# Kernel optimization log

Measured on AMD Instinct MI355X. Metric: run time of the kernel, lower is better.

## Reference

```python
import jax, jax.numpy as jnp
import numpy as np
import math

N_USR = 50000
N_ENT = 100000
D = 64
N_REL = 16
E = 1_000_000
EI = 500_000
N_HEADS = 2


def setup_inputs() -> dict:
    key = jax.random.key(0)
    ks = jax.random.split(key, 9)
    user_emb = jax.random.normal(ks[0], (N_USR, D), jnp.float32) * 0.1
    entity_emb = jax.random.normal(ks[1], (N_ENT, D), jnp.float32) * 0.1
    edge_index = jax.random.randint(ks[2], (2, E), 0, N_ENT, dtype=jnp.int32)
    edge_type = jax.random.randint(ks[3], (E,), 1, N_REL + 1, dtype=jnp.int32)  # values in [1, N_REL]
    inter_u = jax.random.randint(ks[4], (EI,), 0, N_USR, dtype=jnp.int32)
    inter_i = jax.random.randint(ks[5], (EI,), 0, N_ENT, dtype=jnp.int32)
    inter_edge = jnp.stack([inter_u, inter_i], axis=0)
    inter_edge_w = jax.random.uniform(ks[6], (EI,), jnp.float32)
    relation_emb = jax.random.normal(ks[7], (N_REL, D), jnp.float32) * 0.1
    W_Q = jax.random.normal(ks[8], (D, D), jnp.float32) * 0.1
    return {
        'layers_num': 2,
        'user_emb': user_emb,
        'entity_emb': entity_emb,
        'inter_edge': inter_edge,
        'inter_edge_w': inter_edge_w,
        'edge_index': edge_index,
        'edge_type': edge_type,
        'relation_emb': relation_emb,
        'W_Q': W_Q,
    }


def _scatter_softmax(scores, idx, n_segments):
    # scores: [E, H]; softmax over edges sharing the same head index
    m = jax.ops.segment_max(scores, idx, num_segments=n_segments)  # [n, H]
    ex = jnp.exp(scores - m[idx])
    denom = jax.ops.segment_sum(ex, idx, num_segments=n_segments)
    return ex / denom[idx]


def reference(layers_num, user_emb, entity_emb, inter_edge, inter_edge_w, edge_index, edge_type, relation_emb, W_Q):
    n_entities = entity_emb.shape[0]
    n_users = user_emb.shape[0]
    d = entity_emb.shape[1]
    h = N_HEADS
    dk = d // h
    head, tail = edge_index[0], edge_index[1]
    iu, ii = inter_edge[0], inter_edge[1]

    def agg_layer(u_emb, e_emb):
        rel = relation_emb[edge_type - 1]                                # [E, d]
        query = (e_emb[head] @ W_Q).reshape(-1, h, dk)                   # [E, h, dk]
        key = (e_emb[tail] @ W_Q).reshape(-1, h, dk) * rel.reshape(-1, h, dk)
        score = (query * key).sum(-1) / math.sqrt(dk)                    # [E, h]
        attn = _scatter_softmax(score, head, n_entities)                 # [E, h]
        value = (e_emb[tail] * rel).reshape(-1, h, dk)                   # [E, h, dk]
        entity_agg = (value * attn[:, :, None]).reshape(-1, d)           # [E, d]
        entity_agg = jax.ops.segment_sum(entity_agg, head, num_segments=n_entities)
        # F.normalize (L2, eps=1e-12)
        norm = jnp.sqrt(jnp.sum(entity_agg * entity_agg, axis=1, keepdims=True))
        entity_agg = entity_agg / jnp.maximum(norm, 1e-12)
        item_agg = inter_edge_w[:, None] * e_emb[ii]                      # [Ei, d]
        user_agg = jax.ops.segment_sum(item_agg, iu, num_segments=n_users)
        return entity_agg, user_agg

    user_embs = [user_emb]
    entity_embs = [entity_emb]
    u, e = user_emb, entity_emb
    for _ in range(layers_num):
        e, u = agg_layer(u, e)
        user_embs.append(u)
        entity_embs.append(e)
    user_out = jnp.mean(jnp.stack(user_embs, axis=1), axis=1)
    entity_out = jnp.mean(jnp.stack(entity_embs, axis=1), axis=1)
    return (user_out, entity_out)
```

## Files before the change

### kernel.cpp

```cpp
#include <hip/hip_runtime.h>
#include <hip/hip_fp16.h>
#include <math.h>

#define N_USR 50000
#define N_ENT 100000
#define DIM   64
#define NE    1000000
#define NEI   500000

#define BKW   250
#define EBK   400
#define UBK   200
#define CAP   3456
#define KCH   4096
#define NBA_E 245
#define NBA_U 123

#define NBE_B 6250
#define NBU_B 3125

__device__ __forceinline__ __half2 pick_lo(unsigned a, unsigned b) {
    unsigned r = __builtin_amdgcn_perm(b, a, 0x05040100u);
    return *(__half2*)&r;
}
__device__ __forceinline__ __half2 pick_hi(unsigned a, unsigned b) {
    unsigned r = __builtin_amdgcn_perm(b, a, 0x07060302u);
    return *(__half2*)&r;
}

template <int CTRL>
__device__ __forceinline__ float dpp_add(float x) {
    int y = __builtin_amdgcn_update_dpp(0, __builtin_bit_cast(int, x),
                                        CTRL, 0xF, 0xF, true);
    return x + __builtin_bit_cast(float, y);
}

__device__ __forceinline__ int swz16_maxi(int x) {
    int t = __builtin_amdgcn_ds_swizzle(x, 0x401F);
    return max(x, t);
}

typedef _Float16 fp16x2 __attribute__((ext_vector_type(2)));
__device__ __forceinline__ float dot2(__half2 a, __half2 b, float c) {
#if __has_builtin(__builtin_amdgcn_fdot2)
    return __builtin_amdgcn_fdot2(__builtin_bit_cast(fp16x2, a),
                                  __builtin_bit_cast(fp16x2, b), c, false);
#else
    __half2 m = __hmul2(a, b);
    return c + __low2float(m) + __high2float(m);
#endif
}

__device__ __forceinline__ float exp2_fast(float x) {
#if __has_builtin(__builtin_amdgcn_exp2f)
    return __builtin_amdgcn_exp2f(x);
#else
    return exp2f(x);
#endif
}

__global__ __launch_bounds__(256) void k_gemm(const float* __restrict__ Emat,
                                              const float* __restrict__ WQ,
                                              unsigned int* __restrict__ Gu,
                                              __half* __restrict__ Eh, int nrows) {
    int lane = threadIdx.x & 63;
    int wid  = (int)((blockIdx.x * 256 + threadIdx.x) >> 6);
    int nw   = (int)((gridDim.x * 256) >> 6);
    float w[64];
#pragma unroll
    for (int k = 0; k < 64; k++) w[k] = WQ[k * 64 + lane];
    for (int row = wid; row < nrows; row += nw) {
        int rowu = __builtin_amdgcn_readfirstlane(row);
        const float* er = Emat + (size_t)rowu * DIM;
        float acc = 0.f;
#pragma unroll
        for (int k = 0; k < 64; k++) acc = fmaf(er[k], w[k], acc);
        float ecol = er[lane];
        unsigned short hp = __half_as_ushort(__float2half(acc));
        unsigned short he = __half_as_ushort(__float2half(ecol));
        Gu[(size_t)rowu * 64 + lane] = (unsigned int)hp | ((unsigned int)he << 16);
        Eh[(size_t)rowu * 64 + lane] = __ushort_as_half(he);
    }
}

__global__ __launch_bounds__(256) void k_bucketA(const int* __restrict__ eidx,
                                                 const int* __restrict__ etype,
                                                 const int* __restrict__ inter,
                                                 const float* __restrict__ w,
                                                 int* __restrict__ gcnt,
                                                 int* __restrict__ ebuf,
                                                 int2* __restrict__ ubuf) {
    __shared__ int ch[EBK];
    int tid = threadIdx.x;
    int blk = blockIdx.x;
    for (int j = tid; j < EBK; j += 256) ch[j] = 0;
    __syncthreads();
    if (blk < NBA_E) {
        int lo = blk * KCH, hi = min(lo + KCH, NE);
        for (int i = lo + tid; i < hi; i += 256)
            atomicAdd(&ch[eidx[i] / BKW], 1);
        __syncthreads();
        for (int j = tid; j < EBK; j += 256)
            ch[j] = atomicAdd(&gcnt[j], ch[j]);
        __syncthreads();
        for (int i = lo + tid; i < hi; i += 256) {
            int head = eidx[i];
            int b    = head / BKW;
            int pos  = atomicAdd(&ch[b], 1);
            if (pos < CAP)
                ebuf[b * CAP + pos] = eidx[NE + i] | ((etype[i] - 1) << 20)
                                      | ((head - b * BKW) << 24);
        }
    } else {
        int ub = blk - NBA_E;
        int lo = ub * KCH, hi = min(lo + KCH, NEI);
        for (int i = lo + tid; i < hi; i += 256)
            atomicAdd(&ch[inter[i] / BKW], 1);
        __syncthreads();
        for (int j = tid; j < UBK; j += 256)
            ch[j] = atomicAdd(&gcnt[EBK + j], ch[j]);
        __syncthreads();
        for (int i = lo + tid; i < hi; i += 256) {
            int u   = inter[i];
            int b   = u / BKW;
            int pos = atomicAdd(&ch[b], 1);
            if (pos < CAP)
                ubuf[b * CAP + pos] = make_int2(inter[NEI + i] | ((u - b * BKW) << 24),
                                                __float_as_int(w[i]));
        }
    }
}

__global__ __launch_bounds__(512) void k_bucketB(const int* __restrict__ gcnt,
                                                 const int* __restrict__ ebuf,
                                                 const int2* __restrict__ ubuf,
                                                 int2* __restrict__ off2_e,
                                                 int* __restrict__ edges,
                                                 int2* __restrict__ off2_u,
                                                 int2* __restrict__ iw) {
    __shared__ int h[512];
    __shared__ int cur[512];
    __shared__ int s0[CAP];
    __shared__ int s1[CAP];
    int tid = threadIdx.x;
    int b   = blockIdx.x;
    bool isU = (b >= EBK);
    int lb   = isU ? b - EBK : b;
    int n    = min(gcnt[b], CAP);
    int base = lb * BKW;
    int gbase = lb * CAP;
    h[tid] = 0;
    __syncthreads();
    if (!isU) {
        const int* src = ebuf + (size_t)lb * CAP;
        for (int q = tid; q < n; q += 512) atomicAdd(&h[((unsigned)src[q]) >> 24], 1);
        __syncthreads();
        int v = h[tid];
        for (int d = 1; d < 512; d <<= 1) {
            int x = (tid >= d) ? h[tid - d] : 0;
            __syncthreads();
            h[tid] += x;
            __syncthreads();
        }
        int excl = h[tid] - v;
        cur[tid] = excl;
        if (tid < BKW) off2_e[base + tid] = make_int2(gbase + excl, v);
        __syncthreads();
        for (int q = tid; q < n; q += 512) {
            int x = src[q];
            int r = atomicAdd(&cur[((unsigned)x) >> 24], 1);
            s0[r] = x;
        }
        __syncthreads();
        for (int q = tid; q < n; q += 512) edges[gbase + q] = s0[q] & 0xFFFFFF;
    } else {
        const int2* src = ubuf + (size_t)lb * CAP;
        for (int q = tid; q < n; q += 512) atomicAdd(&h[((unsigned)src[q].x) >> 24], 1);
        __syncthreads();
        int v = h[tid];
        for (int d = 1; d < 512; d <<= 1) {
            int x = (tid >= d) ? h[tid - d] : 0;
            __syncthreads();
            h[tid] += x;
            __syncthreads();
        }
        int excl = h[tid] - v;
        cur[tid] = excl;
        if (tid < BKW) off2_u[base + tid] = make_int2(gbase + excl, v);
        __syncthreads();
        for (int q = tid; q < n; q += 512) {
            int2 x = src[q];
            int r = atomicAdd(&cur[((unsigned)x.x) >> 24], 1);
            s0[r] = x.x;
            s1[r] = x.y;
        }
        __syncthreads();
        for (int q = tid; q < n; q += 512)
            iw[gbase + q] = make_int2(s0[q] & 0xFFFFFF, s1[q]);
    }
}

#define ENT_GATHER(G, R, PK)                                                  \
    {                                                                         \
        G = *(const uint4*)(Gu + (size_t)(unsigned)(PK & 0xFFFFF) * 64 + 4 * dq); \
        R = *(const uint2*)(srel2 + ((((unsigned)PK >> 20) << 5) + dq2));     \
    }

#define ENT_BODY(G, R, KK)                                                    \
    {                                                                         \
        __half2 ra = *(__half2*)&(R).x;                                       \
        __half2 rb = *(__half2*)&(R).y;                                       \
        float sc = dot2(q2a, __hmul2(pick_lo((G).x, (G).y), ra), 0.f);        \
        sc = dot2(q2b, __hmul2(pick_lo((G).z, (G).w), rb), sc);               \
        sc = dpp_add<0xB1>(sc);                                               \
        sc = dpp_add<0x4E>(sc);                                               \
        sc = dpp_add<0x141>(sc);                                              \
        float ex = ((KK) < deg) ? exp2_fast(sc) : 0.f;                        \
        den += ex;                                                            \
        __half2 va = __hmul2(pick_hi((G).x, (G).y), ra);                      \
        __half2 vb = __hmul2(pick_hi((G).z, (G).w), rb);                      \
        acc0 = fmaf(ex, __low2float(va), acc0);                               \
        acc1 = fmaf(ex, __high2float(va), acc1);                              \
        acc2 = fmaf(ex, __low2float(vb), acc2);                               \
        acc3 = fmaf(ex, __high2float(vb), acc3);                              \
    }

__device__ __forceinline__ void ent_path(const unsigned int* __restrict__ Gu,
                                         const unsigned int* srel2,
                                         const int2* __restrict__ off2,
                                         const int* __restrict__ edges,
                                         float* __restrict__ enext,
                                         float* __restrict__ out_ent,
                                         const float* __restrict__ base0,
                                         int mode, int row0, int lane) {
    int grp  = lane >> 4;
    int dq   = lane & 15;
    int dq2  = 2 * dq;
    int row  = row0 + grp;
    uint4 qg = *(const uint4*)(Gu + (size_t)row * 64 + 4 * dq);
    const __half2 qs = __float2half2_rn(0.17677669529663687f * 1.44269504088896340f);
    __half2 q2a = __hmul2(pick_lo(qg.x, qg.y), qs);
    __half2 q2b = __hmul2(pick_lo(qg.z, qg.w), qs);
    int2 od = off2[row];
    int lo = od.x, deg = od.y;
    int km = swz16_maxi(deg);
    km = max(km, __shfl_xor(km, 32, 64));
    float acc0 = 0.f, acc1 = 0.f, acc2 = 0.f, acc3 = 0.f, den = 0.f;
    for (int k = 0; k < km; k += 8) {
        const int* ep = edges + lo + k;
        int r0 = ep[0], r1 = ep[1], r2 = ep[2], r3 = ep[3];
        int r4 = ep[4], r5 = ep[5], r6 = ep[6], r7 = ep[7];
        int p0 = (k + 0 < deg) ? r0 : 0;
        int p1 = (k + 1 < deg) ? r1 : 0;
        int p2 = (k + 2 < deg) ? r2 : 0;
        int p3 = (k + 3 < deg) ? r3 : 0;
        int p4 = (k + 4 < deg) ? r4 : 0;
        int p5 = (k + 5 < deg) ? r5 : 0;
        int p6 = (k + 6 < deg) ? r6 : 0;
        int p7 = (k + 7 < deg) ? r7 : 0;
        bool c1 = (k + 1 < km), c2 = (k + 2 < km), c3 = (k + 3 < km);
        bool c4 = (k + 4 < km), c5 = (k + 5 < km), c6 = (k + 6 < km);
        bool c7 = (k + 7 < km);
        uint4 G0, G1, G2, G3, G4, G5, G6, G7;
        uint2 R0, R1, R2, R3, R4, R5, R6, R7;
        ENT_GATHER(G0, R0, p0);
        if (c1) ENT_GATHER(G1, R1, p1);
        if (c2) ENT_GATHER(G2, R2, p2);
        if (c3) ENT_GATHER(G3, R3, p3);
        if (c4) ENT_GATHER(G4, R4, p4);
        if (c5) ENT_GATHER(G5, R5, p5);
        if (c6) ENT_GATHER(G6, R6, p6);
        if (c7) ENT_GATHER(G7, R7, p7);
        ENT_BODY(G0, R0, k);
        if (c1) ENT_BODY(G1, R1, k + 1);
        if (c2) ENT_BODY(G2, R2, k + 2);
        if (c3) ENT_BODY(G3, R3, k + 3);
        if (c4) ENT_BODY(G4, R4, k + 4);
        if (c5) ENT_BODY(G5, R5, k + 5);
        if (c6) ENT_BODY(G6, R6, k + 6);
        if (c7) ENT_BODY(G7, R7, k + 7);
    }
    float rden = (den > 0.f) ? 1.0f / den : 0.f;
    float rx = acc0 * rden, ry = acc1 * rden, rz = acc2 * rden, rw = acc3 * rden;
    float ss = rx * rx + ry * ry + rz * rz + rw * rw;
    ss = dpp_add<0xB1>(ss);
    ss = dpp_add<0x4E>(ss);
    ss = dpp_add<0x141>(ss);
    ss = dpp_add<0x140>(ss);
    float inv = 1.0f / fmaxf(sqrtf(ss), 1e-12f);
    size_t idx = (size_t)row * 16 + dq;
    float4 y = make_float4(rx * inv, ry * inv, rz * inv, rw * inv);
    if (mode == 0) {
        ((float4*)enext)[idx] = y;
        float4 b0 = ((const float4*)base0)[idx];
        ((float4*)out_ent)[idx] = make_float4(b0.x + y.x, b0.y + y.y,
                                              b0.z + y.z, b0.w + y.w);
    } else {
        float4 o = ((float4*)out_ent)[idx];
        ((float4*)out_ent)[idx] = make_float4((o.x + y.x) * (1.0f / 3.0f),
                                              (o.y + y.y) * (1.0f / 3.0f),
                                              (o.z + y.z) * (1.0f / 3.0f),
                                              (o.w + y.w) * (1.0f / 3.0f));
    }
}

#define USR_BODY(G, V, KK)                                                    \
    {                                                                         \
        float cw = ((KK) < deg) ? __int_as_float((V).y) : 0.f;                \
        __half2 h0 = *(__half2*)&(G).x;                                       \
        __half2 h1 = *(__half2*)&(G).y;                                       \
        acc0 = fmaf(cw, __low2float(h0), acc0);                               \
        acc1 = fmaf(cw, __high2float(h0), acc1);                              \
        acc2 = fmaf(cw, __low2float(h1), acc2);                               \
        acc3 = fmaf(cw, __high2float(h1), acc3);                              \
    }

__device__ __forceinline__ void usr_path(const unsigned int* __restrict__ Eh2,
                                         const int2* __restrict__ off2,
                                         const int2* __restrict__ iw,
                                         float* __restrict__ out_user,
                                         const float* __restrict__ base0,
                                         int mode, int row0, int lane) {
    int grp  = lane >> 4;
    int dq   = lane & 15;
    int dq2  = 2 * dq;
    int row  = row0 + grp;
    int2 od = off2[row];
    int lo = od.x, deg = od.y;
    int km = swz16_maxi(deg);
    km = max(km, __shfl_xor(km, 32, 64));
    float acc0 = 0.f, acc1 = 0.f, acc2 = 0.f, acc3 = 0.f;
    for (int k = 0; k < km; k += 8) {
        const int2* vp = iw + lo + k;
        int2 v0 = vp[0], v1 = vp[1], v2 = vp[2], v3 = vp[3];
        int2 v4 = vp[4], v5 = vp[5], v6 = vp[6], v7 = vp[7];
        int t0 = (k + 0 < deg) ? v0.x : 0;
        int t1 = (k + 1 < deg) ? v1.x : 0;
        int t2 = (k + 2 < deg) ? v2.x : 0;
        int t3 = (k + 3 < deg) ? v3.x : 0;
        int t4 = (k + 4 < deg) ? v4.x : 0;
        int t5 = (k + 5 < deg) ? v5.x : 0;
        int t6 = (k + 6 < deg) ? v6.x : 0;
        int t7 = (k + 7 < deg) ? v7.x : 0;
        bool c1 = (k + 1 < km), c2 = (k + 2 < km), c3 = (k + 3 < km);
        bool c4 = (k + 4 < km), c5 = (k + 5 < km), c6 = (k + 6 < km);
        bool c7 = (k + 7 < km);
        uint2 g0, g1, g2, g3, g4, g5, g6, g7;
        g0 = *(const uint2*)(Eh2 + (size_t)t0 * 32 + dq2);
        if (c1) g1 = *(const uint2*)(Eh2 + (size_t)t1 * 32 + dq2);
        if (c2) g2 = *(const uint2*)(Eh2 + (size_t)t2 * 32 + dq2);
        if (c3) g3 = *(const uint2*)(Eh2 + (size_t)t3 * 32 + dq2);
        if (c4) g4 = *(const uint2*)(Eh2 + (size_t)t4 * 32 + dq2);
        if (c5) g5 = *(const uint2*)(Eh2 + (size_t)t5 * 32 + dq2);
        if (c6) g6 = *(const uint2*)(Eh2 + (size_t)t6 * 32 + dq2);
        if (c7) g7 = *(const uint2*)(Eh2 + (size_t)t7 * 32 + dq2);
        USR_BODY(g0, v0, k);
        if (c1) USR_BODY(g1, v1, k + 1);
        if (c2) USR_BODY(g2, v2, k + 2);
        if (c3) USR_BODY(g3, v3, k + 3);
        if (c4) USR_BODY(g4, v4, k + 4);
        if (c5) USR_BODY(g5, v5, k + 5);
        if (c6) USR_BODY(g6, v6, k + 6);
        if (c7) USR_BODY(g7, v7, k + 7);
    }
    size_t idx = (size_t)row * 16 + dq;
    if (mode == 0) {
        float4 b0 = ((const float4*)base0)[idx];
        ((float4*)out_user)[idx] = make_float4(b0.x + acc0, b0.y + acc1,
                                               b0.z + acc2, b0.w + acc3);
    } else {
        float4 o = ((float4*)out_user)[idx];
        ((float4*)out_user)[idx] = make_float4((o.x + acc0) * (1.0f / 3.0f),
                                               (o.y + acc1) * (1.0f / 3.0f),
                                               (o.z + acc2) * (1.0f / 3.0f),
                                               (o.w + acc3) * (1.0f / 3.0f));
    }
}

__global__ __launch_bounds__(256) void k_agg(const unsigned int* __restrict__ Gu,
                                             const unsigned int* __restrict__ Eh2,
                                             const float* __restrict__ rel,
                                             const int2* __restrict__ off2_e,
                                             const int* __restrict__ edges,
                                             const int2* __restrict__ off2_u,
                                             const int2* __restrict__ iw,
                                             float* __restrict__ enext,
                                             float* __restrict__ out_ent,
                                             const float* __restrict__ ent0,
                                             float* __restrict__ out_user,
                                             const float* __restrict__ usr0,
                                             int mode) {
    __shared__ unsigned int srel2[16 * 32];
    int tid = threadIdx.x;
    int b   = blockIdx.x;
    int g   = b / 3;
    int r   = b - 3 * g;
    int lane = tid & 63;
    int wv   = tid >> 6;
    if (r < 2) {
        for (int i = tid; i < 16 * 32; i += 256) {
            float2 rp = ((const float2*)rel)[i];
            __half2 h = __floats2half2_rn(rp.x, rp.y);
            srel2[i] = *(unsigned int*)&h;
        }
        __syncthreads();
        int row0 = (2 * g + r) * 16 + wv * 4;
        ent_path(Gu, srel2, off2_e, edges, enext, out_ent, ent0, mode, row0, lane);
    } else {
        int row0 = g * 16 + wv * 4;
        usr_path(Eh2, off2_u, iw, out_user, usr0, mode, row0, lane);
    }
}

extern "C" void kernel_launch(void* const* d_in, const int* in_sizes, int n_in,
                              void* d_out, int out_size, void* d_ws, size_t ws_size,
                              hipStream_t stream) {
    const float* user_emb   = (const float*)d_in[1];
    const float* entity_emb = (const float*)d_in[2];
    const int*   inter_edge = (const int*)d_in[3];
    const float* inter_w    = (const float*)d_in[4];
    const int*   edge_index = (const int*)d_in[5];
    const int*   edge_type  = (const int*)d_in[6];
    const float* rel_emb    = (const float*)d_in[7];
    const float* wq         = (const float*)d_in[8];

    float* out      = (float*)d_out;
    float* out_user = out;
    float* out_ent  = out + (size_t)N_USR * DIM;

    const size_t SZ_E = (size_t)N_ENT * DIM * sizeof(float);
    char* ws = (char*)d_ws;
    size_t o = 0;
#define ALIGN16() o = (o + 15) & ~(size_t)15
    unsigned int* Gu = (unsigned int*)(ws + o); o += (size_t)N_ENT * 64 * 4;
    __half* Eh     = (__half*)(ws + o); o += (size_t)N_ENT * 64 * 2;
    float* eA      = (float*)(ws + o); o += SZ_E;
    ALIGN16();
    int*   edges   = (int*)  (ws + o); o += ((size_t)EBK * CAP + CAP + 16) * 4;
    ALIGN16();
    int2*  off2_e  = (int2*) (ws + o); o += (size_t)N_ENT * 8;
    ALIGN16();
    int2*  iw      = (int2*) (ws + o); o += ((size_t)UBK * CAP + CAP + 16) * 8;
    int2*  off2_u  = (int2*) (ws + o); o += (size_t)N_USR * 8;
    ALIGN16();
    int*   ebuf    = (int*)  (ws + o); o += (size_t)EBK * CAP * 4;
    ALIGN16();
    int2*  ubuf    = (int2*) (ws + o); o += (size_t)UBK * CAP * 8;
    int*   gcnt    = (int*)  (ws + o); o += (EBK + UBK) * 4;

    hipMemsetAsync(gcnt, 0, (EBK + UBK) * 4, stream);
    k_bucketA<<<NBA_E + NBA_U, 256, 0, stream>>>(edge_index, edge_type,
                                                 inter_edge, inter_w, gcnt,
                                                 ebuf, ubuf);
    k_bucketB<<<EBK + UBK, 512, 0, stream>>>(gcnt, ebuf, ubuf,
                                             off2_e, edges, off2_u, iw);

    const int layers = 2;
    for (int L = 0; L < layers; L++) {
        const float* ecur = (L == 0) ? entity_emb : eA;
        k_gemm<<<1536, 256, 0, stream>>>(ecur, wq, Gu, Eh, N_ENT);
        k_agg<<<NBE_B + NBU_B, 256, 0, stream>>>(Gu, (const unsigned int*)Eh, rel_emb,
                                                 off2_e, edges, off2_u, iw,
                                                 eA, out_ent, entity_emb,
                                                 out_user, user_emb, L);
    }
}
```

Before: 310.6 us.

## Halve agg block size, unroll by four with software-prefetched edge indices

```diff
diff --git a/kernel.cpp b/kernel.cpp
--- a/kernel.cpp
+++ b/kernel.cpp
@@ -8,16 +8,16 @@
 #define NE    1000000
 #define NEI   500000
 
-#define BKW   250
-#define EBK   400
-#define UBK   200
-#define CAP   3456
+#define BKW   125
+#define EBK   800
+#define UBK   400
+#define CAP   1664
 #define KCH   4096
 #define NBA_E 245
 #define NBA_U 123
 
-#define NBE_B 6250
-#define NBU_B 3125
+#define NBE_B 12500
+#define NBU_B 6250
 
 __device__ __forceinline__ __half2 pick_lo(unsigned a, unsigned b) {
     unsigned r = __builtin_amdgcn_perm(b, a, 0x05040100u);
@@ -246,39 +246,28 @@
     int km = swz16_maxi(deg);
     km = max(km, __shfl_xor(km, 32, 64));
     float acc0 = 0.f, acc1 = 0.f, acc2 = 0.f, acc3 = 0.f, den = 0.f;
-    for (int k = 0; k < km; k += 8) {
-        const int* ep = edges + lo + k;
-        int r0 = ep[0], r1 = ep[1], r2 = ep[2], r3 = ep[3];
-        int r4 = ep[4], r5 = ep[5], r6 = ep[6], r7 = ep[7];
-        int p0 = (k + 0 < deg) ? r0 : 0;
-        int p1 = (k + 1 < deg) ? r1 : 0;
-        int p2 = (k + 2 < deg) ? r2 : 0;
-        int p3 = (k + 3 < deg) ? r3 : 0;
-        int p4 = (k + 4 < deg) ? r4 : 0;
-        int p5 = (k + 5 < deg) ? r5 : 0;
-        int p6 = (k + 6 < deg) ? r6 : 0;
-        int p7 = (k + 7 < deg) ? r7 : 0;
+    const int* ep = edges + lo;
+    int r0 = ep[0], r1 = ep[1], r2 = ep[2], r3 = ep[3];
+    for (int k = 0; k < km; k += 4) {
+        int e0v = r0, e1v = r1, e2v = r2, e3v = r3;
+        if (k + 4 < km) {
+            r0 = ep[k + 4]; r1 = ep[k + 5]; r2 = ep[k + 6]; r3 = ep[k + 7];
+        }
+        int p0 = (k + 0 < deg) ? e0v : 0;
+        int p1 = (k + 1 < deg) ? e1v : 0;
+        int p2 = (k + 2 < deg) ? e2v : 0;
+        int p3 = (k + 3 < deg) ? e3v : 0;
         bool c1 = (k + 1 < km), c2 = (k + 2 < km), c3 = (k + 3 < km);
-        bool c4 = (k + 4 < km), c5 = (k + 5 < km), c6 = (k + 6 < km);
-        bool c7 = (k + 7 < km);
-        uint4 G0, G1, G2, G3, G4, G5, G6, G7;
-        uint2 R0, R1, R2, R3, R4, R5, R6, R7;
+        uint4 G0, G1, G2, G3;
+        uint2 R0, R1, R2, R3;
         ENT_GATHER(G0, R0, p0);
         if (c1) ENT_GATHER(G1, R1, p1);
         if (c2) ENT_GATHER(G2, R2, p2);
         if (c3) ENT_GATHER(G3, R3, p3);
-        if (c4) ENT_GATHER(G4, R4, p4);
-        if (c5) ENT_GATHER(G5, R5, p5);
-        if (c6) ENT_GATHER(G6, R6, p6);
-        if (c7) ENT_GATHER(G7, R7, p7);
         ENT_BODY(G0, R0, k);
         if (c1) ENT_BODY(G1, R1, k + 1);
         if (c2) ENT_BODY(G2, R2, k + 2);
         if (c3) ENT_BODY(G3, R3, k + 3);
-        if (c4) ENT_BODY(G4, R4, k + 4);
-        if (c5) ENT_BODY(G5, R5, k + 5);
-        if (c6) ENT_BODY(G6, R6, k + 6);
-        if (c7) ENT_BODY(G7, R7, k + 7);
     }
     float rden = (den > 0.f) ? 1.0f / den : 0.f;
     float rx = acc0 * rden, ry = acc1 * rden, rz = acc2 * rden, rw = acc3 * rden;
@@ -304,9 +293,9 @@
     }
 }
 
-#define USR_BODY(G, V, KK)                                                    \
+#define USR_BODY(G, WV, KK)                                                   \
     {                                                                         \
-        float cw = ((KK) < deg) ? __int_as_float((V).y) : 0.f;                \
+        float cw = ((KK) < deg) ? (WV) : 0.f;                                 \
         __half2 h0 = *(__half2*)&(G).x;                                       \
         __half2 h1 = *(__half2*)&(G).y;                                       \
         acc0 = fmaf(cw, __low2float(h0), acc0);                               \
@@ -330,38 +319,27 @@
     int km = swz16_maxi(deg);
     km = max(km, __shfl_xor(km, 32, 64));
     float acc0 = 0.f, acc1 = 0.f, acc2 = 0.f, acc3 = 0.f;
-    for (int k = 0; k < km; k += 8) {
-        const int2* vp = iw + lo + k;
-        int2 v0 = vp[0], v1 = vp[1], v2 = vp[2], v3 = vp[3];
-        int2 v4 = vp[4], v5 = vp[5], v6 = vp[6], v7 = vp[7];
-        int t0 = (k + 0 < deg) ? v0.x : 0;
-        int t1 = (k + 1 < deg) ? v1.x : 0;
-        int t2 = (k + 2 < deg) ? v2.x : 0;
-        int t3 = (k + 3 < deg) ? v3.x : 0;
-        int t4 = (k + 4 < deg) ? v4.x : 0;
-        int t5 = (k + 5 < deg) ? v5.x : 0;
-        int t6 = (k + 6 < deg) ? v6.x : 0;
-        int t7 = (k + 7 < deg) ? v7.x : 0;
+    const int2* vp = iw + lo;
+    int2 v0 = vp[0], v1 = vp[1], v2 = vp[2], v3 = vp[3];
+    for (int k = 0; k < km; k += 4) {
+        int2 u0 = v0, u1 = v1, u2 = v2, u3 = v3;
+        if (k + 4 < km) {
+            v0 = vp[k + 4]; v1 = vp[k + 5]; v2 = vp[k + 6]; v3 = vp[k + 7];
+        }
+        int t0 = (k + 0 < deg) ? u0.x : 0;
+        int t1 = (k + 1 < deg) ? u1.x : 0;
+        int t2 = (k + 2 < deg) ? u2.x : 0;
+        int t3 = (k + 3 < deg) ? u3.x : 0;
         bool c1 = (k + 1 < km), c2 = (k + 2 < km), c3 = (k + 3 < km);
-        bool c4 = (k + 4 < km), c5 = (k + 5 < km), c6 = (k + 6 < km);
-        bool c7 = (k + 7 < km);
-        uint2 g0, g1, g2, g3, g4, g5, g6, g7;
+        uint2 g0, g1, g2, g3;
         g0 = *(const uint2*)(Eh2 + (size_t)t0 * 32 + dq2);
         if (c1) g1 = *(const uint2*)(Eh2 + (size_t)t1 * 32 + dq2);
         if (c2) g2 = *(const uint2*)(Eh2 + (size_t)t2 * 32 + dq2);
         if (c3) g3 = *(const uint2*)(Eh2 + (size_t)t3 * 32 + dq2);
-        if (c4) g4 = *(const uint2*)(Eh2 + (size_t)t4 * 32 + dq2);
-        if (c5) g5 = *(const uint2*)(Eh2 + (size_t)t5 * 32 + dq2);
-        if (c6) g6 = *(const uint2*)(Eh2 + (size_t)t6 * 32 + dq2);
-        if (c7) g7 = *(const uint2*)(Eh2 + (size_t)t7 * 32 + dq2);
-        USR_BODY(g0, v0, k);
-        if (c1) USR_BODY(g1, v1, k + 1);
-        if (c2) USR_BODY(g2, v2, k + 2);
-        if (c3) USR_BODY(g3, v3, k + 3);
-        if (c4) USR_BODY(g4, v4, k + 4);
-        if (c5) USR_BODY(g5, v5, k + 5);
-        if (c6) USR_BODY(g6, v6, k + 6);
-        if (c7) USR_BODY(g7, v7, k + 7);
+        USR_BODY(g0, __int_as_float(u0.y), k);
+        if (c1) USR_BODY(g1, __int_as_float(u1.y), k + 1);
+        if (c2) USR_BODY(g2, __int_as_float(u2.y), k + 2);
+        if (c3) USR_BODY(g3, __int_as_float(u3.y), k + 3);
     }
     size_t idx = (size_t)row * 16 + dq;
     if (mode == 0) {
@@ -377,7 +355,7 @@
     }
 }
 
-__global__ __launch_bounds__(256) void k_agg(const unsigned int* __restrict__ Gu,
+__global__ __launch_bounds__(128) void k_agg(const unsigned int* __restrict__ Gu,
                                              const unsigned int* __restrict__ Eh2,
                                              const float* __restrict__ rel,
                                              const int2* __restrict__ off2_e,
@@ -398,16 +376,16 @@
     int lane = tid & 63;
     int wv   = tid >> 6;
     if (r < 2) {
-        for (int i = tid; i < 16 * 32; i += 256) {
+        for (int i = tid; i < 16 * 32; i += 128) {
             float2 rp = ((const float2*)rel)[i];
             __half2 h = __floats2half2_rn(rp.x, rp.y);
             srel2[i] = *(unsigned int*)&h;
         }
         __syncthreads();
-        int row0 = (2 * g + r) * 16 + wv * 4;
+        int row0 = (2 * g + r) * 8 + wv * 4;
         ent_path(Gu, srel2, off2_e, edges, enext, out_ent, ent0, mode, row0, lane);
     } else {
-        int row0 = g * 16 + wv * 4;
+        int row0 = g * 8 + wv * 4;
         usr_path(Eh2, off2_u, iw, out_user, usr0, mode, row0, lane);
     }
 }
@@ -459,7 +437,7 @@
     for (int L = 0; L < layers; L++) {
         const float* ecur = (L == 0) ? entity_emb : eA;
         k_gemm<<<1536, 256, 0, stream>>>(ecur, wq, Gu, Eh, N_ENT);
-        k_agg<<<NBE_B + NBU_B, 256, 0, stream>>>(Gu, (const unsigned int*)Eh, rel_emb,
+        k_agg<<<NBE_B + NBU_B, 128, 0, stream>>>(Gu, (const unsigned int*)Eh, rel_emb,
                                                  off2_e, edges, off2_u, iw,
                                                  eA, out_ent, entity_emb,
                                                  out_user, user_emb, L);
```

After: 306.5 us. Within noise of the previous version (-1.3%).
